# Performance work log

Hardware: AMD Instinct MI355X
Metric: run time of the kernel (lower is better)

The kernel has to match this reference:

```python
import jax, jax.numpy as jnp
import numpy as np

D_MODEL = 1024
N_HEADS = 16
N_GROUPS = 4
HEAD_DIM = D_MODEL // N_HEADS          # 64
HPG = N_HEADS // N_GROUPS              # heads per group = 4
KV_DIM = N_GROUPS * HEAD_DIM           # 256


def setup_inputs() -> dict:
    key = jax.random.key(0)
    ks = jax.random.split(key, 9)
    B, T = 2, 2048
    s = 0.02
    return {
        "x":  jax.random.normal(ks[0], (B, T, D_MODEL), dtype=jnp.float32),
        "Wq": jax.random.normal(ks[1], (D_MODEL, D_MODEL), dtype=jnp.float32) * s,
        "bq": jnp.zeros((D_MODEL,), dtype=jnp.float32),
        "Wk": jax.random.normal(ks[2], (D_MODEL, KV_DIM), dtype=jnp.float32) * s,
        "bk": jnp.zeros((KV_DIM,), dtype=jnp.float32),
        "Wv": jax.random.normal(ks[3], (D_MODEL, KV_DIM), dtype=jnp.float32) * s,
        "bv": jnp.zeros((KV_DIM,), dtype=jnp.float32),
        "Wo": jax.random.normal(ks[4], (D_MODEL, D_MODEL), dtype=jnp.float32) * s,
        "bo": jnp.zeros((D_MODEL,), dtype=jnp.float32),
    }


def reference(x, Wq, bq, Wk, bk, Wv, bv, Wo, bo):
    B, T, C = x.shape
    q = x @ Wq + bq                                   # [B,T,C]
    k = x @ Wk + bk                                   # [B,T,G*hd]
    v = x @ Wv + bv

    # [B, G, hpg, T, hd] for q; [B, G, T, hd] for k,v (native GQA head sharing,
    # equivalent to repeat_interleave on the group dim in the torch code)
    q = q.reshape(B, T, N_GROUPS, HPG, HEAD_DIM).transpose(0, 2, 3, 1, 4)
    k = k.reshape(B, T, N_GROUPS, HEAD_DIM).transpose(0, 2, 1, 3)
    v = v.reshape(B, T, N_GROUPS, HEAD_DIM).transpose(0, 2, 1, 3)

    scale = 1.0 / jnp.sqrt(jnp.float32(HEAD_DIM))
    attn = jnp.einsum('bghqd,bgkd->bghqk', q, k) * scale   # [B,G,hpg,T,T]

    causal = jnp.tril(jnp.ones((T, T), dtype=bool))        # True = keep
    attn = jnp.where(causal, attn, jnp.float32(-jnp.inf))
    attn = jax.nn.softmax(attn, axis=-1)
    # dropout p=0.1 only in training mode; reference is eval mode (identity)

    out = jnp.einsum('bghqk,bgkd->bghqd', attn, v)         # [B,G,hpg,T,hd]
    out = out.transpose(0, 3, 1, 2, 4).reshape(B, T, C)
    return out @ Wo + bo
```

## Files before the change

### kernel.cpp

```cpp
#include <hip/hip_runtime.h>
#include <hip/hip_bf16.h>
#include <stdint.h>

#define D_MODEL 1024
#define T_LEN   2048
#define BATCH   2
#define N_HEADS 16
#define KV_DIM  256
#define QKV_N   1536
#define M_ROWS  (BATCH * T_LEN)

typedef unsigned short u16;
typedef __bf16 bf16x8 __attribute__((ext_vector_type(8)));
typedef __bf16 bf16x2 __attribute__((ext_vector_type(2)));
typedef float  f32x4  __attribute__((ext_vector_type(4)));

__device__ __forceinline__ u16 f2b(float f) {
    uint32_t u = __builtin_bit_cast(uint32_t, f);
    u += 0x7FFFu + ((u >> 16) & 1u);
    return (u16)(u >> 16);
}

__device__ __forceinline__ uint32_t pk_bf16(float a, float b) {
#if __has_builtin(__builtin_amdgcn_cvt_pk_bf16_f32)
    bf16x2 v = __builtin_amdgcn_cvt_pk_bf16_f32(a, b);
    return __builtin_bit_cast(uint32_t, v);
#else
    return (uint32_t)f2b(a) | ((uint32_t)f2b(b) << 16);
#endif
}

__device__ __forceinline__ void gl_lds16(const void* g, void* l) {
    __builtin_amdgcn_global_load_lds(g, l, 16, 0, 0);
}

__global__ __launch_bounds__(256) void prep(
    const float* __restrict__ x,
    const float* __restrict__ Wq, const float* __restrict__ Wk,
    const float* __restrict__ Wv, const float* __restrict__ Wo,
    u16* __restrict__ xb, u16* __restrict__ WcatT, u16* __restrict__ WoT)
{
    __shared__ u16 tile[32][33];
    int id = blockIdx.x;
    int tid = threadIdx.x;
    if (id < 2048) {
        int i = (id * 256 + tid) * 8;
        float4 a = *(const float4*)&x[i];
        float4 c = *(const float4*)&x[i + 4];
        u16 r[8] = { f2b(a.x), f2b(a.y), f2b(a.z), f2b(a.w),
                     f2b(c.x), f2b(c.y), f2b(c.z), f2b(c.w) };
        *(uint4*)&xb[i] = *(const uint4*)r;
        return;
    }
    int t = id - 2048;
    int bx = t % 80;
    int k0 = (t / 80) * 32;
    const float* src; u16* dst; int N, n0;
    if (bx < 32)       { src = Wq; dst = WcatT;                   N = 1024; n0 = bx * 32; }
    else if (bx < 40)  { src = Wk; dst = WcatT + 1024 * 1024;     N = 256;  n0 = (bx - 32) * 32; }
    else if (bx < 48)  { src = Wv; dst = WcatT + 1280 * 1024;     N = 256;  n0 = (bx - 40) * 32; }
    else               { src = Wo; dst = WoT;                     N = 1024; n0 = (bx - 48) * 32; }
    for (int i = 0; i < 4; ++i) {
        int idx = tid + i * 256;
        int r = idx >> 5, c = idx & 31;
        tile[r][c] = f2b(src[(size_t)(k0 + r) * N + (n0 + c)]);
    }
    __syncthreads();
    for (int i = 0; i < 4; ++i) {
        int idx = tid + i * 256;
        int r = idx >> 5, c = idx & 31;
        dst[(size_t)(n0 + r) * 1024 + (k0 + c)] = tile[c][r];
    }
}

__global__ __launch_bounds__(256) void gemm_qkv(
    const u16* __restrict__ A, const u16* __restrict__ BT,
    const float* __restrict__ bq, const float* __restrict__ bk,
    const float* __restrict__ bv, u16* __restrict__ Qb,
    u16* __restrict__ Kpack, u16* __restrict__ Vpack)
{
    constexpr int K = 1024;
    constexpr float SCALE = 0.125f * 1.44269504088896f;
    __shared__ __align__(16) u16 As[64 * 64];
    __shared__ __align__(16) u16 Bs[128 * 64];

    int tid  = threadIdx.x;
    int lane = tid & 63, w = tid >> 6;
    int quad = lane >> 4, l15 = lane & 15;
    int m0 = blockIdx.y * 64, n0 = blockIdx.x * 128;
    int lr = lane >> 3, lc = (lane & 7) * 8;

    f32x4 acc[4][2] = {};

    for (int k0 = 0; k0 < K; k0 += 64) {
        for (int t = 0; t < 2; ++t) {
            int rb = t * 32 + w * 8;
            gl_lds16(&A[(size_t)(m0 + rb + lr) * K + k0 + lc], &As[rb * 64]);
        }
        for (int t = 0; t < 4; ++t) {
            int rb = t * 32 + w * 8;
            gl_lds16(&BT[(size_t)(n0 + rb + lr) * K + k0 + lc], &Bs[rb * 64]);
        }
        __syncthreads();
        for (int kk = 0; kk < 64; kk += 32) {
            bf16x8 a[4], b[2];
            for (int i = 0; i < 4; ++i)
                a[i] = *(const bf16x8*)&As[(i * 16 + l15) * 64 + kk + quad * 8];
            for (int j = 0; j < 2; ++j)
                b[j] = *(const bf16x8*)&Bs[(w * 32 + j * 16 + l15) * 64 + kk + quad * 8];
            for (int i = 0; i < 4; ++i)
                for (int j = 0; j < 2; ++j)
                    acc[i][j] = __builtin_amdgcn_mfma_f32_16x16x32_bf16(
                        a[i], b[j], acc[i][j], 0, 0, 0);
        }
        __syncthreads();
    }

    for (int j = 0; j < 2; ++j) {
        int col = n0 + w * 32 + j * 16 + l15;
        float bj = (col < 1024) ? bq[col] : (col < 1280) ? bk[col - 1024] : bv[col - 1280];
        for (int i = 0; i < 4; ++i) {
            int rowb = m0 + i * 16 + quad * 4;
            int bb = rowb >> 11, keyloc = rowb & 2047;
            int t64 = keyloc >> 6;
            if (col < 1024) {
                for (int r = 0; r < 4; ++r)
                    Qb[(size_t)(rowb + r) * 1024 + col] =
                        f2b((acc[i][j][r] + bj) * SCALE);
            } else if (col < 1280) {
                int d = col - 1024; int g = d >> 6; d &= 63;
                int kk = d >> 5, qd = (d >> 3) & 3, e = d & 7;
                int ntk = (keyloc >> 4) & 3, l15k = keyloc & 15;
                size_t base = ((((size_t)(bb * 4 + g) * 32 + t64) * 2 + kk) * 4
                               + ntk) * 512 + qd * 128 + l15k * 8 + e;
                for (int r = 0; r < 4; ++r)
                    Kpack[base + r * 8] = f2b(acc[i][j][r] + bj);
            } else {
                int d = col - 1280; int g = d >> 6; d &= 63;
                int dt = d >> 4, l15v = d & 15;
                int kkp = (keyloc >> 5) & 1, qv = (keyloc >> 3) & 3, e0 = keyloc & 7;
                u16 tmp[4];
                for (int r = 0; r < 4; ++r) tmp[r] = f2b(acc[i][j][r] + bj);
                size_t base = ((((size_t)(bb * 4 + g) * 32 + t64) * 2 + kkp) * 4
                               + dt) * 512 + (qv * 16 + l15v) * 8 + e0;
                *(uint64_t*)&Vpack[base] = *(const uint64_t*)tmp;
            }
        }
    }
}

__global__ __launch_bounds__(256) void gemm_out(
    const u16* __restrict__ A, const u16* __restrict__ BT,
    const float* __restrict__ bias, float* __restrict__ C)
{
    constexpr int K = 1024, N = 1024;
    __shared__ __align__(16) u16 As[64 * 64];
    __shared__ __align__(16) u16 Bs[128 * 64];

    int tid  = threadIdx.x;
    int lane = tid & 63, w = tid >> 6;
    int quad = lane >> 4, l15 = lane & 15;
    int m0 = blockIdx.y * 64, n0 = blockIdx.x * 128;
    int lr = lane >> 3, lc = (lane & 7) * 8;

    f32x4 acc[4][2] = {};

    for (int k0 = 0; k0 < K; k0 += 64) {
        for (int t = 0; t < 2; ++t) {
            int rb = t * 32 + w * 8;
            gl_lds16(&A[(size_t)(m0 + rb + lr) * K + k0 + lc], &As[rb * 64]);
        }
        for (int t = 0; t < 4; ++t) {
            int rb = t * 32 + w * 8;
            gl_lds16(&BT[(size_t)(n0 + rb + lr) * K + k0 + lc], &Bs[rb * 64]);
        }
        __syncthreads();
        for (int kk = 0; kk < 64; kk += 32) {
            bf16x8 a[4], b[2];
            for (int i = 0; i < 4; ++i)
                a[i] = *(const bf16x8*)&As[(i * 16 + l15) * 64 + kk + quad * 8];
            for (int j = 0; j < 2; ++j)
                b[j] = *(const bf16x8*)&Bs[(w * 32 + j * 16 + l15) * 64 + kk + quad * 8];
            for (int i = 0; i < 4; ++i)
                for (int j = 0; j < 2; ++j)
                    acc[i][j] = __builtin_amdgcn_mfma_f32_16x16x32_bf16(
                        a[i], b[j], acc[i][j], 0, 0, 0);
        }
        __syncthreads();
    }

    for (int j = 0; j < 2; ++j) {
        int col = n0 + w * 32 + j * 16 + l15;
        float bj = bias[col];
        for (int i = 0; i < 4; ++i) {
            int rowb = m0 + i * 16 + quad * 4;
            for (int r = 0; r < 4; ++r)
                C[(size_t)(rowb + r) * N + col] = acc[i][j][r] + bj;
        }
    }
}

__global__ __launch_bounds__(256, 4) void attn_kernel(
    const u16* __restrict__ Qb,
    const u16* __restrict__ Kpack,
    const u16* __restrict__ Vpack,
    u16* __restrict__ AO)
{
    constexpr int LDP = 72;
    __shared__ __align__(16) u16 Ps[4][32 * LDP];

    int tid  = threadIdx.x;
    int lane = tid & 63, w = tid >> 6;
    int quad = lane >> 4, l15 = lane & 15;

    int gid = blockIdx.x;
    int b = gid & 1, g = (gid >> 1) & 3;
    int j = 63 - (gid >> 3);
    int head = g * 4 + w;
    int q0 = j * 32;
    int iters = (j >> 1) + 1;

    const u16* Qp = Qb + ((size_t)b * T_LEN + q0) * 1024 + head * 64;
    const u16* Kp = Kpack + (size_t)(b * 4 + g) * 131072 + (size_t)lane * 8;
    const u16* Vp = Vpack + (size_t)(b * 4 + g) * 131072 + (size_t)lane * 8;
    u16*       Op = AO + ((size_t)b * T_LEN + q0) * D_MODEL + head * 64;
    u16* Pw = Ps[w];

    bf16x8 Qfrag[2][2];
    #pragma unroll
    for (int ntq = 0; ntq < 2; ++ntq)
        #pragma unroll
        for (int kk = 0; kk < 2; ++kk)
            Qfrag[ntq][kk] = *(const bf16x8*)
                &Qp[(size_t)(ntq * 16 + l15) * 1024 + kk * 32 + quad * 8];

    f32x4 o[2][4] = {};
    float lsum[2] = {0.f, 0.f};

    for (int tg = 0; tg < iters; ++tg) {
        bool diag = (tg == iters - 1);

        const u16* kb = Kp + (size_t)tg * 4096;
        bf16x8 aK[2][4];
        #pragma unroll
        for (int kk = 0; kk < 2; ++kk)
            #pragma unroll
            for (int ntk = 0; ntk < 4; ++ntk)
                aK[kk][ntk] = *(const bf16x8*)(kb + (kk * 4 + ntk) * 512);

        #pragma unroll
        for (int ntq = 0; ntq < 2; ++ntq) {
            f32x4 s[4] = {};
            #pragma unroll
            for (int kk = 0; kk < 2; ++kk) {
                bf16x8 bQ = Qfrag[ntq][kk];
                #pragma unroll
                for (int ntk = 0; ntk < 4; ++ntk)
                    s[ntk] = __builtin_amdgcn_mfma_f32_16x16x32_bf16(
                        aK[kk][ntk], bQ, s[ntk], 0, 0, 0);
            }
            int qrow = q0 + ntq * 16 + l15;
            float lacc = 0.f;
            #pragma unroll
            for (int ntk = 0; ntk < 4; ++ntk) {
                float p0, p1, p2, p3;
                if (diag) {
                    int key = tg * 64 + ntk * 16 + quad * 4;
                    p0 = (key + 0 <= qrow) ? exp2f(s[ntk][0]) : 0.f;
                    p1 = (key + 1 <= qrow) ? exp2f(s[ntk][1]) : 0.f;
                    p2 = (key + 2 <= qrow) ? exp2f(s[ntk][2]) : 0.f;
                    p3 = (key + 3 <= qrow) ? exp2f(s[ntk][3]) : 0.f;
                } else {
                    p0 = exp2f(s[ntk][0]);
                    p1 = exp2f(s[ntk][1]);
                    p2 = exp2f(s[ntk][2]);
                    p3 = exp2f(s[ntk][3]);
                }
                lacc += (p0 + p1) + (p2 + p3);
                uint2 pv;
                pv.x = pk_bf16(p0, p1);
                pv.y = pk_bf16(p2, p3);
                *(uint2*)&Pw[(ntq * 16 + l15) * LDP + ntk * 16 + quad * 4] = pv;
            }
            lsum[ntq] += lacc;
        }

        const u16* vb = Vp + (size_t)tg * 4096;
        #pragma unroll
        for (int kkp = 0; kkp < 2; ++kkp) {
            bf16x8 bV[4];
            #pragma unroll
            for (int dt = 0; dt < 4; ++dt)
                bV[dt] = *(const bf16x8*)(vb + (kkp * 4 + dt) * 512);
            #pragma unroll
            for (int ntq = 0; ntq < 2; ++ntq) {
                bf16x8 aP = *(const bf16x8*)
                    &Pw[(ntq * 16 + l15) * LDP + kkp * 32 + quad * 8];
                #pragma unroll
                for (int dt = 0; dt < 4; ++dt)
                    o[ntq][dt] = __builtin_amdgcn_mfma_f32_16x16x32_bf16(
                        aP, bV[dt], o[ntq][dt], 0, 0, 0);
            }
        }
    }

    #pragma unroll
    for (int ntq = 0; ntq < 2; ++ntq) {
        float l = lsum[ntq];
        l += __shfl_xor(l, 16, 64);
        l += __shfl_xor(l, 32, 64);
        float linv = 1.0f / l;
        float li[4];
        #pragma unroll
        for (int r = 0; r < 4; ++r)
            li[r] = __shfl(linv, quad * 4 + r, 64);
        #pragma unroll
        for (int dt = 0; dt < 4; ++dt)
            #pragma unroll
            for (int r = 0; r < 4; ++r)
                Op[(size_t)(ntq * 16 + quad * 4 + r) * D_MODEL + dt * 16 + l15] =
                    f2b(o[ntq][dt][r] * li[r]);
    }
}

extern "C" void kernel_launch(void* const* d_in, const int* in_sizes, int n_in,
                              void* d_out, int out_size, void* d_ws, size_t ws_size,
                              hipStream_t stream) {
    const float* x  = (const float*)d_in[0];
    const float* Wq = (const float*)d_in[1];
    const float* bq = (const float*)d_in[2];
    const float* Wk = (const float*)d_in[3];
    const float* bk = (const float*)d_in[4];
    const float* Wv = (const float*)d_in[5];
    const float* bv = (const float*)d_in[6];
    const float* Wo = (const float*)d_in[7];
    const float* bo = (const float*)d_in[8];
    float* out = (float*)d_out;

    u16* ws    = (u16*)d_ws;
    u16* xb    = ws;  ws += (size_t)M_ROWS * 1024;
    u16* WcatT = ws;  ws += (size_t)QKV_N * 1024;
    u16* WoT   = ws;  ws += 1024 * 1024;
    u16* Qb    = ws;  ws += (size_t)M_ROWS * 1024;
    u16* Kpack = ws;  ws += (size_t)M_ROWS * KV_DIM;
    u16* Vpack = ws;  ws += (size_t)M_ROWS * KV_DIM;
    u16* AO    = xb;

    prep<<<2048 + 2560, 256, 0, stream>>>(x, Wq, Wk, Wv, Wo, xb, WcatT, WoT);
    gemm_qkv<<<dim3(QKV_N / 128, M_ROWS / 64), 256, 0, stream>>>(
        xb, WcatT, bq, bk, bv, Qb, Kpack, Vpack);
    attn_kernel<<<512, 256, 0, stream>>>(Qb, Kpack, Vpack, AO);
    gemm_out<<<dim3(1024 / 128, M_ROWS / 64), 256, 0, stream>>>(AO, WoT, bo, out);
}
```

Before: 192.7 us.

## Enlarge GEMM tiles to 128x128 and halve attention query tile to 16 rows

Both projection GEMMs move from 64x128 to 128x128 block tiles with a 2x2 warp layout, so each wave computes a 64x64 sub-tile and loads more operand fragments per MFMA. The attention kernel now handles 16 query rows per block instead of 32, doubling the grid to 1024 blocks. The causal work ordering is also changed to interleave long and short query tiles for better load balance. The aim is better operand reuse in the GEMMs and higher parallelism and balance in attention. The cost is fewer GEMM blocks and more accumulator registers, and attention re-reads K and V more often per query row.

```diff
diff --git a/kernel.cpp b/kernel.cpp
--- a/kernel.cpp
+++ b/kernel.cpp
@@ -81,46 +81,44 @@
 {
     constexpr int K = 1024;
     constexpr float SCALE = 0.125f * 1.44269504088896f;
-    __shared__ __align__(16) u16 As[64 * 64];
+    __shared__ __align__(16) u16 As[128 * 64];
     __shared__ __align__(16) u16 Bs[128 * 64];
 
     int tid  = threadIdx.x;
     int lane = tid & 63, w = tid >> 6;
     int quad = lane >> 4, l15 = lane & 15;
-    int m0 = blockIdx.y * 64, n0 = blockIdx.x * 128;
+    int wr = w >> 1, wc = w & 1;
+    int m0 = blockIdx.y * 128, n0 = blockIdx.x * 128;
     int lr = lane >> 3, lc = (lane & 7) * 8;
 
-    f32x4 acc[4][2] = {};
+    f32x4 acc[4][4] = {};
 
     for (int k0 = 0; k0 < K; k0 += 64) {
-        for (int t = 0; t < 2; ++t) {
+        for (int t = 0; t < 4; ++t) {
             int rb = t * 32 + w * 8;
             gl_lds16(&A[(size_t)(m0 + rb + lr) * K + k0 + lc], &As[rb * 64]);
-        }
-        for (int t = 0; t < 4; ++t) {
-            int rb = t * 32 + w * 8;
             gl_lds16(&BT[(size_t)(n0 + rb + lr) * K + k0 + lc], &Bs[rb * 64]);
         }
         __syncthreads();
         for (int kk = 0; kk < 64; kk += 32) {
-            bf16x8 a[4], b[2];
+            bf16x8 a[4], b[4];
             for (int i = 0; i < 4; ++i)
-                a[i] = *(const bf16x8*)&As[(i * 16 + l15) * 64 + kk + quad * 8];
-            for (int j = 0; j < 2; ++j)
-                b[j] = *(const bf16x8*)&Bs[(w * 32 + j * 16 + l15) * 64 + kk + quad * 8];
+                a[i] = *(const bf16x8*)&As[(wr * 64 + i * 16 + l15) * 64 + kk + quad * 8];
+            for (int j = 0; j < 4; ++j)
+                b[j] = *(const bf16x8*)&Bs[(wc * 64 + j * 16 + l15) * 64 + kk + quad * 8];
             for (int i = 0; i < 4; ++i)
-                for (int j = 0; j < 2; ++j)
+                for (int j = 0; j < 4; ++j)
                     acc[i][j] = __builtin_amdgcn_mfma_f32_16x16x32_bf16(
                         a[i], b[j], acc[i][j], 0, 0, 0);
         }
         __syncthreads();
     }
 
-    for (int j = 0; j < 2; ++j) {
-        int col = n0 + w * 32 + j * 16 + l15;
+    for (int j = 0; j < 4; ++j) {
+        int col = n0 + wc * 64 + j * 16 + l15;
         float bj = (col < 1024) ? bq[col] : (col < 1280) ? bk[col - 1024] : bv[col - 1280];
         for (int i = 0; i < 4; ++i) {
-            int rowb = m0 + i * 16 + quad * 4;
+            int rowb = m0 + wr * 64 + i * 16 + quad * 4;
             int bb = rowb >> 11, keyloc = rowb & 2047;
             int t64 = keyloc >> 6;
             if (col < 1024) {
@@ -154,46 +152,44 @@
     const float* __restrict__ bias, float* __restrict__ C)
 {
     constexpr int K = 1024, N = 1024;
-    __shared__ __align__(16) u16 As[64 * 64];
+    __shared__ __align__(16) u16 As[128 * 64];
     __shared__ __align__(16) u16 Bs[128 * 64];
 
     int tid  = threadIdx.x;
     int lane = tid & 63, w = tid >> 6;
     int quad = lane >> 4, l15 = lane & 15;
-    int m0 = blockIdx.y * 64, n0 = blockIdx.x * 128;
+    int wr = w >> 1, wc = w & 1;
+    int m0 = blockIdx.y * 128, n0 = blockIdx.x * 128;
     int lr = lane >> 3, lc = (lane & 7) * 8;
 
-    f32x4 acc[4][2] = {};
+    f32x4 acc[4][4] = {};
 
     for (int k0 = 0; k0 < K; k0 += 64) {
-        for (int t = 0; t < 2; ++t) {
+        for (int t = 0; t < 4; ++t) {
             int rb = t * 32 + w * 8;
             gl_lds16(&A[(size_t)(m0 + rb + lr) * K + k0 + lc], &As[rb * 64]);
-        }
-        for (int t = 0; t < 4; ++t) {
-            int rb = t * 32 + w * 8;
             gl_lds16(&BT[(size_t)(n0 + rb + lr) * K + k0 + lc], &Bs[rb * 64]);
         }
         __syncthreads();
         for (int kk = 0; kk < 64; kk += 32) {
-            bf16x8 a[4], b[2];
+            bf16x8 a[4], b[4];
             for (int i = 0; i < 4; ++i)
-                a[i] = *(const bf16x8*)&As[(i * 16 + l15) * 64 + kk + quad * 8];
-            for (int j = 0; j < 2; ++j)
-                b[j] = *(const bf16x8*)&Bs[(w * 32 + j * 16 + l15) * 64 + kk + quad * 8];
+                a[i] = *(const bf16x8*)&As[(wr * 64 + i * 16 + l15) * 64 + kk + quad * 8];
+            for (int j = 0; j < 4; ++j)
+                b[j] = *(const bf16x8*)&Bs[(wc * 64 + j * 16 + l15) * 64 + kk + quad * 8];
             for (int i = 0; i < 4; ++i)
-                for (int j = 0; j < 2; ++j)
+                for (int j = 0; j < 4; ++j)
                     acc[i][j] = __builtin_amdgcn_mfma_f32_16x16x32_bf16(
                         a[i], b[j], acc[i][j], 0, 0, 0);
         }
         __syncthreads();
     }
 
-    for (int j = 0; j < 2; ++j) {
-        int col = n0 + w * 32 + j * 16 + l15;
+    for (int j = 0; j < 4; ++j) {
+        int col = n0 + wc * 64 + j * 16 + l15;
         float bj = bias[col];
         for (int i = 0; i < 4; ++i) {
-            int rowb = m0 + i * 16 + quad * 4;
+            int rowb = m0 + wr * 64 + i * 16 + quad * 4;
             for (int r = 0; r < 4; ++r)
                 C[(size_t)(rowb + r) * N + col] = acc[i][j][r] + bj;
         }
@@ -207,7 +203,7 @@
     u16* __restrict__ AO)
 {
     constexpr int LDP = 72;
-    __shared__ __align__(16) u16 Ps[4][32 * LDP];
+    __shared__ __align__(16) u16 Ps[4][16 * LDP];
 
     int tid  = threadIdx.x;
     int lane = tid & 63, w = tid >> 6;
@@ -215,10 +211,13 @@
 
     int gid = blockIdx.x;
     int b = gid & 1, g = (gid >> 1) & 3;
-    int j = 63 - (gid >> 3);
+    int s = gid >> 3;
+    int kq = s >> 5, tq = s & 31;
+    int q4 = (kq & 1) ? tq : (31 - tq);
+    int j  = q4 * 4 + kq;
     int head = g * 4 + w;
-    int q0 = j * 32;
-    int iters = (j >> 1) + 1;
+    int q0 = j * 16;
+    int iters = q4 + 1;
 
     const u16* Qp = Qb + ((size_t)b * T_LEN + q0) * 1024 + head * 64;
     const u16* Kp = Kpack + (size_t)(b * 4 + g) * 131072 + (size_t)lane * 8;
@@ -226,16 +225,13 @@
     u16*       Op = AO + ((size_t)b * T_LEN + q0) * D_MODEL + head * 64;
     u16* Pw = Ps[w];
 
-    bf16x8 Qfrag[2][2];
+    bf16x8 Qfrag[2];
     #pragma unroll
-    for (int ntq = 0; ntq < 2; ++ntq)
-        #pragma unroll
-        for (int kk = 0; kk < 2; ++kk)
-            Qfrag[ntq][kk] = *(const bf16x8*)
-                &Qp[(size_t)(ntq * 16 + l15) * 1024 + kk * 32 + quad * 8];
-
-    f32x4 o[2][4] = {};
-    float lsum[2] = {0.f, 0.f};
+    for (int kk = 0; kk < 2; ++kk)
+        Qfrag[kk] = *(const bf16x8*)&Qp[(size_t)l15 * 1024 + kk * 32 + quad * 8];
+
+    f32x4 o[4] = {};
+    float lsum = 0.f;
 
     for (int tg = 0; tg < iters; ++tg) {
         bool diag = (tg == iters - 1);
@@ -248,42 +244,39 @@
             for (int ntk = 0; ntk < 4; ++ntk)
                 aK[kk][ntk] = *(const bf16x8*)(kb + (kk * 4 + ntk) * 512);
 
-        #pragma unroll
-        for (int ntq = 0; ntq < 2; ++ntq) {
-            f32x4 s[4] = {};
+        f32x4 sacc[4] = {};
+        #pragma unroll
+        for (int kk = 0; kk < 2; ++kk) {
+            bf16x8 bQ = Qfrag[kk];
             #pragma unroll
-            for (int kk = 0; kk < 2; ++kk) {
-                bf16x8 bQ = Qfrag[ntq][kk];
-                #pragma unroll
-                for (int ntk = 0; ntk < 4; ++ntk)
-                    s[ntk] = __builtin_amdgcn_mfma_f32_16x16x32_bf16(
-                        aK[kk][ntk], bQ, s[ntk], 0, 0, 0);
+            for (int ntk = 0; ntk < 4; ++ntk)
+                sacc[ntk] = __builtin_amdgcn_mfma_f32_16x16x32_bf16(
+                    aK[kk][ntk], bQ, sacc[ntk], 0, 0, 0);
+        }
+        int qrow = q0 + l15;
+        float lacc = 0.f;
+        #pragma unroll
+        for (int ntk = 0; ntk < 4; ++ntk) {
+            float p0, p1, p2, p3;
+            if (diag) {
+                int key = tg * 64 + ntk * 16 + quad * 4;
+                p0 = (key + 0 <= qrow) ? exp2f(sacc[ntk][0]) : 0.f;
+                p1 = (key + 1 <= qrow) ? exp2f(sacc[ntk][1]) : 0.f;
+                p2 = (key + 2 <= qrow) ? exp2f(sacc[ntk][2]) : 0.f;
+                p3 = (key + 3 <= qrow) ? exp2f(sacc[ntk][3]) : 0.f;
+            } else {
+                p0 = exp2f(sacc[ntk][0]);
+                p1 = exp2f(sacc[ntk][1]);
+                p2 = exp2f(sacc[ntk][2]);
+                p3 = exp2f(sacc[ntk][3]);
             }
-            int qrow = q0 + ntq * 16 + l15;
-            float lacc = 0.f;
-            #pragma unroll
-            for (int ntk = 0; ntk < 4; ++ntk) {
-                float p0, p1, p2, p3;
-                if (diag) {
-                    int key = tg * 64 + ntk * 16 + quad * 4;
-                    p0 = (key + 0 <= qrow) ? exp2f(s[ntk][0]) : 0.f;
-                    p1 = (key + 1 <= qrow) ? exp2f(s[ntk][1]) : 0.f;
-                    p2 = (key + 2 <= qrow) ? exp2f(s[ntk][2]) : 0.f;
-                    p3 = (key + 3 <= qrow) ? exp2f(s[ntk][3]) : 0.f;
-                } else {
-                    p0 = exp2f(s[ntk][0]);
-                    p1 = exp2f(s[ntk][1]);
-                    p2 = exp2f(s[ntk][2]);
-                    p3 = exp2f(s[ntk][3]);
-                }
-                lacc += (p0 + p1) + (p2 + p3);
-                uint2 pv;
-                pv.x = pk_bf16(p0, p1);
-                pv.y = pk_bf16(p2, p3);
-                *(uint2*)&Pw[(ntq * 16 + l15) * LDP + ntk * 16 + quad * 4] = pv;
-            }
-            lsum[ntq] += lacc;
-        }
+            lacc += (p0 + p1) + (p2 + p3);
+            uint2 pv;
+            pv.x = pk_bf16(p0, p1);
+            pv.y = pk_bf16(p2, p3);
+            *(uint2*)&Pw[l15 * LDP + ntk * 16 + quad * 4] = pv;
+        }
+        lsum += lacc;
 
         const u16* vb = Vp + (size_t)tg * 4096;
         #pragma unroll
@@ -292,35 +285,28 @@
             #pragma unroll
             for (int dt = 0; dt < 4; ++dt)
                 bV[dt] = *(const bf16x8*)(vb + (kkp * 4 + dt) * 512);
+            bf16x8 aP = *(const bf16x8*)&Pw[l15 * LDP + kkp * 32 + quad * 8];
             #pragma unroll
-            for (int ntq = 0; ntq < 2; ++ntq) {
-                bf16x8 aP = *(const bf16x8*)
-                    &Pw[(ntq * 16 + l15) * LDP + kkp * 32 + quad * 8];
-                #pragma unroll
-                for (int dt = 0; dt < 4; ++dt)
-                    o[ntq][dt] = __builtin_amdgcn_mfma_f32_16x16x32_bf16(
-                        aP, bV[dt], o[ntq][dt], 0, 0, 0);
-            }
-        }
-    }
-
+            for (int dt = 0; dt < 4; ++dt)
+                o[dt] = __builtin_amdgcn_mfma_f32_16x16x32_bf16(
+                    aP, bV[dt], o[dt], 0, 0, 0);
+        }
+    }
+
+    float l = lsum;
+    l += __shfl_xor(l, 16, 64);
+    l += __shfl_xor(l, 32, 64);
+    float linv = 1.0f / l;
+    float li[4];
     #pragma unroll
-    for (int ntq = 0; ntq < 2; ++ntq) {
-        float l = lsum[ntq];
-        l += __shfl_xor(l, 16, 64);
-        l += __shfl_xor(l, 32, 64);
-        float linv = 1.0f / l;
-        float li[4];
+    for (int r = 0; r < 4; ++r)
+        li[r] = __shfl(linv, quad * 4 + r, 64);
+    #pragma unroll
+    for (int dt = 0; dt < 4; ++dt)
         #pragma unroll
         for (int r = 0; r < 4; ++r)
-            li[r] = __shfl(linv, quad * 4 + r, 64);
-        #pragma unroll
-        for (int dt = 0; dt < 4; ++dt)
-            #pragma unroll
-            for (int r = 0; r < 4; ++r)
-                Op[(size_t)(ntq * 16 + quad * 4 + r) * D_MODEL + dt * 16 + l15] =
-                    f2b(o[ntq][dt][r] * li[r]);
-    }
+            Op[(size_t)(quad * 4 + r) * D_MODEL + dt * 16 + l15] =
+                f2b(o[dt][r] * li[r]);
 }
 
 extern "C" void kernel_launch(void* const* d_in, const int* in_sizes, int n_in,
@@ -347,8 +333,8 @@
     u16* AO    = xb;
 
     prep<<<2048 + 2560, 256, 0, stream>>>(x, Wq, Wk, Wv, Wo, xb, WcatT, WoT);
-    gemm_qkv<<<dim3(QKV_N / 128, M_ROWS / 64), 256, 0, stream>>>(
+    gemm_qkv<<<dim3(QKV_N / 128, M_ROWS / 128), 256, 0, stream>>>(
         xb, WcatT, bq, bk, bv, Qb, Kpack, Vpack);
-    attn_kernel<<<512, 256, 0, stream>>>(Qb, Kpack, Vpack, AO);
-    gemm_out<<<dim3(1024 / 128, M_ROWS / 64), 256, 0, stream>>>(AO, WoT, bo, out);
-}
+    attn_kernel<<<1024, 256, 0, stream>>>(Qb, Kpack, Vpack, AO);
+    gemm_out<<<dim3(1024 / 128, M_ROWS / 128), 256, 0, stream>>>(AO, WoT, bo, out);
+}
```

Measured after the change: 194.4 us. No clear change (+0.9%).
